# Kernel optimization log

Measured on AMD Instinct MI355X. Metric: run time of the kernel, lower is better.

## Reference

```python
import jax, jax.numpy as jnp
from jax import lax
import numpy as np

DIM = 48
HEADS = 2
HIDDEN = 96  # int(dim * 2.0)
EPS_LN = 1e-5
EPS_NORM = 1e-12


def _ln(x, w, b):
    # WithBias LayerNorm over channel dim (dim=1 in NCHW == last dim in b,(hw),c)
    mu = jnp.mean(x, axis=1, keepdims=True)
    var = jnp.var(x, axis=1, keepdims=True)
    return (x - mu) / jnp.sqrt(var + EPS_LN) * w[None, :, None, None] + b[None, :, None, None]


def _conv1x1(x, w, b):
    # w: [O, C, 1, 1]
    return jnp.einsum('bchw,oc->bohw', x, w[:, :, 0, 0]) + b[None, :, None, None]


def _dwconv3(x, w, b):
    # w: [C, 1, 3, 3], groups=C
    y = lax.conv_general_dilated(x, w, (1, 1), 'SAME',
                                 feature_group_count=x.shape[1],
                                 dimension_numbers=('NCHW', 'OIHW', 'NCHW'))
    return y + b[None, :, None, None]


def _l2norm(x):
    n = jnp.sqrt(jnp.sum(x * x, axis=-1, keepdims=True))
    return x / jnp.maximum(n, EPS_NORM)


def setup_inputs() -> dict:
    key = jax.random.key(0)
    ks = jax.random.split(key, 12)
    s = 0.02
    inp = {
        'x': jax.random.normal(ks[0], (2, DIM, 64, 64), jnp.float32),
        'norm1_w': jnp.ones((DIM,), jnp.float32),
        'norm1_b': jnp.zeros((DIM,), jnp.float32),
        'qkv_w': jax.random.normal(ks[1], (DIM * 3, DIM, 1, 1), jnp.float32) * s,
        'qkv_b': jnp.zeros((DIM * 3,), jnp.float32),
        'qkvdw_w': jax.random.normal(ks[2], (DIM * 3, 1, 3, 3), jnp.float32) * s,
        'qkvdw_b': jnp.zeros((DIM * 3,), jnp.float32),
        'temperature': jnp.ones((HEADS, 1, 1), jnp.float32),
        'proj_w': jax.random.normal(ks[3], (DIM, DIM, 1, 1), jnp.float32) * s,
        'proj_b': jnp.zeros((DIM,), jnp.float32),
        'norm2_w': jnp.ones((DIM,), jnp.float32),
        'norm2_b': jnp.zeros((DIM,), jnp.float32),
        'fi_w': jax.random.normal(ks[4], (HIDDEN * 2, DIM, 1, 1), jnp.float32) * s,
        'fi_b': jnp.zeros((HIDDEN * 2,), jnp.float32),
        'fdw_w': jax.random.normal(ks[5], (HIDDEN * 2, 1, 3, 3), jnp.float32) * s,
        'fdw_b': jnp.zeros((HIDDEN * 2,), jnp.float32),
        'fo_w': jax.random.normal(ks[6], (DIM, HIDDEN, 1, 1), jnp.float32) * s,
        'fo_b': jnp.zeros((DIM,), jnp.float32),
    }
    return inp


def _block(x, norm1_w, norm1_b, qkv_w, qkv_b, qkvdw_w, qkvdw_b, temperature,
           proj_w, proj_b, norm2_w, norm2_b, fi_w, fi_b, fdw_w, fdw_b, fo_w, fo_b):
    b, c, h, w = x.shape
    n = h * w
    chead = c // HEADS
    # --- attention branch ---
    xn = _ln(x, norm1_w, norm1_b)
    qkv = _dwconv3(_conv1x1(xn, qkv_w, qkv_b), qkvdw_w, qkvdw_b)
    q, k, v = jnp.split(qkv, 3, axis=1)
    def to_heads(t):  # [b, heads*chead, h, w] -> [b, heads, n, chead]
        return t.reshape(b, HEADS, chead, n).transpose(0, 1, 3, 2)
    q, k, v = to_heads(q), to_heads(k), to_heads(v)
    q = _l2norm(q)
    k = _l2norm(k)
    attn = jnp.einsum('bhnc,bhmc->bhnm', q, k) * temperature[None]
    attn = jax.nn.softmax(attn, axis=-1)
    out = jnp.einsum('bhnm,bhmc->bhnc', attn, v)
    out = out.transpose(0, 1, 3, 2).reshape(b, c, h, w)
    x = x + _conv1x1(out, proj_w, proj_b)
    # --- ffn branch ---
    xn = _ln(x, norm2_w, norm2_b)
    y = _dwconv3(_conv1x1(xn, fi_w, fi_b), fdw_w, fdw_b)
    y1, y2 = jnp.split(y, 2, axis=1)
    y = jax.nn.gelu(y1, approximate=False) * y2
    x = x + _conv1x1(y, fo_w, fo_b)
    return x


def reference(x, norm1_w, norm1_b, qkv_w, qkv_b, qkvdw_w, qkvdw_b, temperature,
              proj_w, proj_b, norm2_w, norm2_b, fi_w, fi_b, fdw_w, fdw_b, fo_w, fo_b):
    return _block(x, norm1_w, norm1_b, qkv_w, qkv_b, qkvdw_w, qkvdw_b, temperature,
                  proj_w, proj_b, norm2_w, norm2_b, fi_w, fi_b, fdw_w, fdw_b, fo_w, fo_b)
```

## Files before the change

kernel.cpp:

```cpp
#include <hip/hip_runtime.h>
#include <hip/hip_bf16.h>
#include <math.h>

#define NPIX 4096
#define NB 2

typedef __attribute__((ext_vector_type(8))) short short8;
typedef __attribute__((ext_vector_type(4))) float floatx4;

static __device__ inline short f2bf(float f) {
    union { float f; unsigned u; } v; v.f = f;
    unsigned r = (v.u + 0x7FFFu + ((v.u >> 16) & 1u)) >> 16;
    return (short)r;
}
static __device__ inline float bf2f(short s) {
    union { unsigned u; float f; } v;
    v.u = ((unsigned)(unsigned short)s) << 16;
    return v.f;
}
static __device__ inline unsigned pk2(float a, float b) {
    __hip_bfloat162 pk = __float22bfloat162_rn(make_float2(a, b));
    return *(unsigned*)&pk;
}

__global__ void k_prepw(const float* __restrict__ qkvw, const float* __restrict__ fiw,
                        const float* __restrict__ fow, const float* __restrict__ projw,
                        short* __restrict__ qkvwbf, short* __restrict__ fiwbf,
                        short* __restrict__ fowbf, short* __restrict__ projwbf) {
    int idx = blockIdx.x * 256 + threadIdx.x;
    if (idx < 144 * 64) {
        int o = idx >> 6, c = idx & 63;
        qkvwbf[idx] = (c < 48) ? f2bf(qkvw[o * 48 + c]) : (short)0;
        return;
    }
    idx -= 144 * 64;
    if (idx < 192 * 64) {
        int o = idx >> 6, c = idx & 63;
        fiwbf[idx] = (c < 48) ? f2bf(fiw[o * 48 + c]) : (short)0;
        return;
    }
    idx -= 192 * 64;
    if (idx < 48 * 96) {
        fowbf[idx] = f2bf(fow[idx]);
        return;
    }
    idx -= 48 * 96;
    if (idx < 48 * 64) {
        int o = idx >> 6, c = idx & 63;
        int h = c >> 5, cc = c & 31;
        projwbf[idx] = (cc < 24) ? f2bf(projw[o * 48 + h * 24 + cc]) : (short)0;
    }
}

__global__ __launch_bounds__(256) void k_qkv_fused(
    const float* __restrict__ xin, const float* __restrict__ n1w, const float* __restrict__ n1b,
    const short* __restrict__ qkvwbf, const float* __restrict__ qkvb,
    const float* __restrict__ dww, const float* __restrict__ dwb,
    const float* __restrict__ temp,
    short* __restrict__ Qbf, short* __restrict__ Kbf, short* __restrict__ Vbf)
{
    int px0 = blockIdx.x * 16;
    int y = blockIdx.y, b = blockIdx.z;
    int t = threadIdx.x;
    int w = t >> 6, lane = t & 63, l15 = lane & 15, quad = lane >> 4;

    __shared__ __align__(16) short xn[64][72];
    __shared__ short qkv[64][148];
    __shared__ float q2[16][148];
    __shared__ float red[4][64], redq[4][64];
    __shared__ float muS[64], rsS[64];
    __shared__ float dwwS[1296], dwbS[144];
    __shared__ short vmask[64];

    for (int u = t; u < 1296; u += 256) dwwS[u] = dww[u];
    if (t < 144) dwbS[t] = dwb[t];

    int pp = t & 63, cg2 = t >> 6;
    int rr = pp / 18, ix = pp - rr * 18;
    int yy = y + rr - 1, xpx = px0 - 1 + ix;
    bool pv = (pp < 54) && ((unsigned)yy < 64u) && ((unsigned)xpx < 64u);
    if (cg2 == 0) vmask[pp] = pv ? (short)1 : (short)0;

    float v[12]; float s = 0.f, sq = 0.f;
    if (pv) {
        size_t pbase = (size_t)(yy * 64 + xpx);
#pragma unroll
        for (int j2 = 0; j2 < 12; j2++) {
            float vv = xin[((size_t)b * 48 + cg2 * 12 + j2) * NPIX + pbase];
            v[j2] = vv; s += vv; sq += vv * vv;
        }
    } else {
#pragma unroll
        for (int j2 = 0; j2 < 12; j2++) v[j2] = 0.f;
    }
    red[cg2][pp] = s; redq[cg2][pp] = sq;
    __syncthreads();
    if (t < 64) {
        float ss = red[0][t] + red[1][t] + red[2][t] + red[3][t];
        float qq = redq[0][t] + redq[1][t] + redq[2][t] + redq[3][t];
        float mu = ss * (1.f / 48.f);
        float var = qq * (1.f / 48.f) - mu * mu;
        muS[t] = mu; rsS[t] = rsqrtf(var + 1e-5f);
    }
    __syncthreads();
    {
        float mu = muS[pp], rs = rsS[pp];
#pragma unroll
        for (int j2 = 0; j2 < 12; j2++) {
            int c = cg2 * 12 + j2;
            xn[pp][c] = f2bf((v[j2] - mu) * rs * n1w[c] + n1b[c]);
        }
        short8 z8 = {};
        if (cg2 == 0) *(short8*)&xn[pp][48] = z8;
        else if (cg2 == 1) *(short8*)&xn[pp][56] = z8;
    }
    __syncthreads();
    floatx4 zf = {0.f, 0.f, 0.f, 0.f};
    for (int job = w; job < 36; job += 4) {
        int pt = job / 9, ot = job % 9;
        short8 a0 = *(const short8*)&xn[pt * 16 + l15][quad * 8];
        short8 a1 = *(const short8*)&xn[pt * 16 + l15][32 + quad * 8];
        const short* wb = qkvwbf + (ot * 16 + l15) * 64;
        short8 b0 = *(const short8*)(wb + quad * 8);
        short8 b1 = *(const short8*)(wb + 32 + quad * 8);
        floatx4 c = __builtin_amdgcn_mfma_f32_16x16x32_bf16(a0, b0, zf, 0, 0, 0);
        c = __builtin_amdgcn_mfma_f32_16x16x32_bf16(a1, b1, c, 0, 0, 0);
        int oc = ot * 16 + l15;
        float bi = qkvb[oc];
#pragma unroll
        for (int r = 0; r < 4; r++) {
            int opp = pt * 16 + quad * 4 + r;
            qkv[opp][oc] = vmask[opp] ? f2bf(c[r] + bi) : (short)0;
        }
    }
    __syncthreads();
    {
        int i = t & 15, g3 = t >> 4;
        for (int cc = 0; cc < 9; cc++) {
            int c = g3 * 9 + cc;
            const float* wp = dwwS + c * 9;
            float acc = dwbS[c];
#pragma unroll
            for (int dy = 0; dy < 3; dy++)
#pragma unroll
                for (int dx = 0; dx < 3; dx++)
                    acc += bf2f(qkv[dy * 18 + i + dx][c]) * wp[dy * 3 + dx];
            q2[i][c] = acc;
        }
    }
    __syncthreads();
    if (t < 128) {
        int i = t & 15, h = (t >> 4) & 1, sel = t >> 5;
        int n = y * 64 + px0 + i;
        int bh = b * 2 + h;
        if (sel < 2) {
            float vv2[24]; float ss = 0.f;
            int base = sel * 48 + h * 24;
#pragma unroll
            for (int c = 0; c < 24; c++) { vv2[c] = q2[i][base + c]; ss += vv2[c] * vv2[c]; }
            float sc = ((sel == 0) ? temp[h] * 1.44269504089f : 1.f) / fmaxf(sqrtf(ss), 1e-12f);
            short qs[32];
#pragma unroll
            for (int c = 0; c < 24; c++) qs[c] = f2bf(vv2[c] * sc);
#pragma unroll
            for (int c = 24; c < 32; c++) qs[c] = 0;
            short* dst = ((sel == 0) ? Qbf : Kbf) + ((size_t)bh * NPIX + n) * 32;
#pragma unroll
            for (int i8 = 0; i8 < 4; i8++) {
                short8 st;
#pragma unroll
                for (int j2 = 0; j2 < 8; j2++) st[j2] = qs[i8 * 8 + j2];
                *(short8*)(dst + i8 * 8) = st;
            }
        } else {
            int half = sel - 2;
            int r5 = n & 31;
            int pos = (r5 < 16) ? ((r5 >> 2) * 8 + (r5 & 3))
                                : (((r5 & 15) >> 2) * 8 + (r5 & 3) + 4);
            int vcol = (n & ~31) + pos;
#pragma unroll
            for (int cc = 0; cc < 12; cc++) {
                int c = half * 12 + cc;
                Vbf[((size_t)bh * 32 + c) * NPIX + vcol] = f2bf(q2[i][96 + h * 24 + c]);
            }
            if (half == 1) {
#pragma unroll
                for (int c = 24; c < 32; c++)
                    Vbf[((size_t)bh * 32 + c) * NPIX + vcol] =
                        (c == 24) ? (short)0x3F80 : (short)0;
            }
        }
    }
}

__global__ __launch_bounds__(1024) void k_attn_mfma2(
    const short* __restrict__ Qbf, const short* __restrict__ Kbf,
    const short* __restrict__ Vbf, short* __restrict__ O)
{
    int qt = blockIdx.x, bh = blockIdx.y;
    int t = threadIdx.x;
    int tg = t & 255, g = t >> 8;
    int wloc = (t >> 6) & 3, lane = t & 63, l15 = lane & 15, quad = lane >> 4;

    __shared__ __align__(16) short tileK[4][2][64][40];
    __shared__ __align__(16) short tileV[4][2][32][72];
    __shared__ float Ocomb[4][64][33];

    int qrow0 = qt * 64 + wloc * 16;
    short8 bq = *(const short8*)(Qbf + ((size_t)bh * NPIX + qrow0 + l15) * 32 + quad * 8);

    int krow = tg >> 2, kseg = tg & 3;
    int vch = tg >> 3, vseg = tg & 7;
    const short* srcK = Kbf + ((size_t)bh * NPIX + krow) * 32 + kseg * 8;
    const short* srcV = Vbf + ((size_t)(bh * 32 + vch)) * NPIX + vseg * 8;

    int key0 = g * 1024;
    *(short8*)&tileK[g][0][krow][kseg * 8] = *(const short8*)(srcK + (size_t)key0 * 32);
    *(short8*)&tileV[g][0][vch][vseg * 8]  = *(const short8*)(srcV + key0);

    floatx4 zf = {0.f, 0.f, 0.f, 0.f};
    floatx4 o0 = zf, o1 = zf;

    const int NKT = 16;
    for (int kt = 0; kt < NKT; kt++) {
        __syncthreads();
        int cur = kt & 1;
        short8 ldK = {}, ldV = {};
        if (kt < NKT - 1) {
            int kabs = key0 + (kt + 1) * 64;
            ldK = *(const short8*)(srcK + (size_t)kabs * 32);
            ldV = *(const short8*)(srcV + kabs);
        }
        short8 ka0 = *(const short8*)&tileK[g][cur][l15][quad * 8];
        short8 ka1 = *(const short8*)&tileK[g][cur][16 + l15][quad * 8];
        short8 ka2 = *(const short8*)&tileK[g][cur][32 + l15][quad * 8];
        short8 ka3 = *(const short8*)&tileK[g][cur][48 + l15][quad * 8];
        floatx4 s0 = __builtin_amdgcn_mfma_f32_16x16x32_bf16(ka0, bq, zf, 0, 0, 0);
        floatx4 s1 = __builtin_amdgcn_mfma_f32_16x16x32_bf16(ka1, bq, zf, 0, 0, 0);
        floatx4 s2 = __builtin_amdgcn_mfma_f32_16x16x32_bf16(ka2, bq, zf, 0, 0, 0);
        floatx4 s3 = __builtin_amdgcn_mfma_f32_16x16x32_bf16(ka3, bq, zf, 0, 0, 0);
        float e0[4], e1[4], e2[4], e3[4];
#pragma unroll
        for (int r = 0; r < 4; r++) {
            e0[r] = exp2f(s0[r]); e1[r] = exp2f(s1[r]);
            e2[r] = exp2f(s2[r]); e3[r] = exp2f(s3[r]);
        }
        short8 p01, p23;
        {
            unsigned* u01 = (unsigned*)&p01;
            unsigned* u23 = (unsigned*)&p23;
            u01[0] = pk2(e0[0], e0[1]); u01[1] = pk2(e0[2], e0[3]);
            u01[2] = pk2(e1[0], e1[1]); u01[3] = pk2(e1[2], e1[3]);
            u23[0] = pk2(e2[0], e2[1]); u23[1] = pk2(e2[2], e2[3]);
            u23[2] = pk2(e3[0], e3[1]); u23[3] = pk2(e3[2], e3[3]);
        }
        short8 va00 = *(const short8*)&tileV[g][cur][l15][quad * 8];
        short8 va01 = *(const short8*)&tileV[g][cur][l15][32 + quad * 8];
        short8 va10 = *(const short8*)&tileV[g][cur][16 + l15][quad * 8];
        short8 va11 = *(const short8*)&tileV[g][cur][16 + l15][32 + quad * 8];
        o0 = __builtin_amdgcn_mfma_f32_16x16x32_bf16(va00, p01, o0, 0, 0, 0);
        o0 = __builtin_amdgcn_mfma_f32_16x16x32_bf16(va01, p23, o0, 0, 0, 0);
        o1 = __builtin_amdgcn_mfma_f32_16x16x32_bf16(va10, p01, o1, 0, 0, 0);
        o1 = __builtin_amdgcn_mfma_f32_16x16x32_bf16(va11, p23, o1, 0, 0, 0);
        if (kt < NKT - 1) {
            *(short8*)&tileK[g][1 - cur][krow][kseg * 8] = ldK;
            *(short8*)&tileV[g][1 - cur][vch][vseg * 8]  = ldV;
        }
    }
    int qi = wloc * 16 + l15;
#pragma unroll
    for (int r = 0; r < 4; r++) {
        Ocomb[g][qi][quad * 4 + r]      = o0[r];
        Ocomb[g][qi][16 + quad * 4 + r] = o1[r];
    }
    __syncthreads();
    {
        int qq = t >> 4, cp = t & 15;
        float l4 = Ocomb[0][qq][24] + Ocomb[1][qq][24] +
                   Ocomb[2][qq][24] + Ocomb[3][qq][24];
        float inv = 1.f / l4;
        float sa = (Ocomb[0][qq][2 * cp] + Ocomb[1][qq][2 * cp] +
                    Ocomb[2][qq][2 * cp] + Ocomb[3][qq][2 * cp]) * inv;
        float sb = (Ocomb[0][qq][2 * cp + 1] + Ocomb[1][qq][2 * cp + 1] +
                    Ocomb[2][qq][2 * cp + 1] + Ocomb[3][qq][2 * cp + 1]) * inv;
        int b = bh >> 1, h = bh & 1;
        int n = qt * 64 + qq;
        *(unsigned*)(O + ((size_t)b * NPIX + n) * 64 + h * 32 + 2 * cp) = pk2(sa, sb);
    }
}

__global__ __launch_bounds__(256) void k_tail_fused(
    const float* __restrict__ xin, const short* __restrict__ O,
    const short* __restrict__ projwbf, const float* __restrict__ projb,
    const float* __restrict__ n2w, const float* __restrict__ n2b,
    const short* __restrict__ fiwbf, const float* __restrict__ fib,
    const float* __restrict__ fdww, const float* __restrict__ fdwb,
    const short* __restrict__ fowbf, const float* __restrict__ fob,
    float* __restrict__ out)
{
    int px0 = blockIdx.x * 16;
    int y = blockIdx.y, b = blockIdx.z;
    int t = threadIdx.x;
    int w = t >> 6, lane = t & 63, l15 = lane & 15, quad = lane >> 4;

    __shared__ float x1s[64][53];
    __shared__ __align__(16) short xn2[64][72];
    __shared__ short ypre[56][196];
    __shared__ __align__(16) short yv[16][104];
    __shared__ float red[4][64], redq[4][64];
    __shared__ float muS[64], rsS[64];
    __shared__ float fdwwS[1728], fdwbS[192];
    __shared__ short vmask[64];
    __shared__ int nidx[64];

    for (int u = t; u < 1728; u += 256) fdwwS[u] = fdww[u];
    if (t < 192) fdwbS[t] = fdwb[t];
    if (t < 64) {
        int rr = t / 18, ix = t - rr * 18;
        int yy = y + rr - 1, xpx = px0 - 1 + ix;
        bool pv = (t < 54) && ((unsigned)yy < 64u) && ((unsigned)xpx < 64u);
        vmask[t] = pv ? (short)1 : (short)0;
        int n = yy * 64 + xpx;
        n = n < 0 ? 0 : (n > 4095 ? 4095 : n);
        nidx[t] = n;
    }
    __syncthreads();

    floatx4 zf = {0.f, 0.f, 0.f, 0.f};
    for (int job = w; job < 12; job += 4) {
        int pt = job / 3, ot = job % 3;
        const short* oa = O + ((size_t)b * NPIX + nidx[pt * 16 + l15]) * 64;
        short8 a0 = *(const short8*)(oa + quad * 8);
        short8 a1 = *(const short8*)(oa + 32 + quad * 8);
        const short* wb = projwbf + (ot * 16 + l15) * 64;
        short8 b0 = *(const short8*)(wb + quad * 8);
        short8 b1 = *(const short8*)(wb + 32 + quad * 8);
        floatx4 c = __builtin_amdgcn_mfma_f32_16x16x32_bf16(a0, b0, zf, 0, 0, 0);
        c = __builtin_amdgcn_mfma_f32_16x16x32_bf16(a1, b1, c, 0, 0, 0);
        int oc = ot * 16 + l15;
        float bi = projb[oc];
#pragma unroll
        for (int r = 0; r < 4; r++) {
            int opp = pt * 16 + quad * 4 + r;
            x1s[opp][oc] = xin[((size_t)b * 48 + oc) * NPIX + nidx[opp]] + c[r] + bi;
        }
    }
    __syncthreads();
    int pp = t & 63, cg2 = t >> 6;
    {
        float v[12]; float s = 0.f, sq = 0.f;
#pragma unroll
        for (int j2 = 0; j2 < 12; j2++) {
            float vv = x1s[pp][cg2 * 12 + j2];
            v[j2] = vv; s += vv; sq += vv * vv;
        }
        red[cg2][pp] = s; redq[cg2][pp] = sq;
        __syncthreads();
        if (t < 64) {
            float ss = red[0][t] + red[1][t] + red[2][t] + red[3][t];
            float qq = redq[0][t] + redq[1][t] + redq[2][t] + redq[3][t];
            float mu = ss * (1.f / 48.f);
            float var = qq * (1.f / 48.f) - mu * mu;
            muS[t] = mu; rsS[t] = rsqrtf(var + 1e-5f);
        }
        __syncthreads();
        float mu = muS[pp], rs = rsS[pp];
#pragma unroll
        for (int j2 = 0; j2 < 12; j2++) {
            int c = cg2 * 12 + j2;
            xn2[pp][c] = f2bf((v[j2] - mu) * rs * n2w[c] + n2b[c]);
        }
        short8 z8 = {};
        if (cg2 == 0) *(short8*)&xn2[pp][48] = z8;
        else if (cg2 == 1) *(short8*)&xn2[pp][56] = z8;
    }
    __syncthreads();
    for (int job = w; job < 48; job += 4) {
        int pt = job / 12, ot = job % 12;
        short8 a0 = *(const short8*)&xn2[pt * 16 + l15][quad * 8];
        short8 a1 = *(const short8*)&xn2[pt * 16 + l15][32 + quad * 8];
        const short* wb = fiwbf + (ot * 16 + l15) * 64;
        short8 b0 = *(const short8*)(wb + quad * 8);
        short8 b1 = *(const short8*)(wb + 32 + quad * 8);
        floatx4 c = __builtin_amdgcn_mfma_f32_16x16x32_bf16(a0, b0, zf, 0, 0, 0);
        c = __builtin_amdgcn_mfma_f32_16x16x32_bf16(a1, b1, c, 0, 0, 0);
        int oc = ot * 16 + l15;
        float bi = fib[oc];
#pragma unroll
        for (int r = 0; r < 4; r++) {
            int opp = pt * 16 + quad * 4 + r;
            if (opp < 56) ypre[opp][oc] = vmask[opp] ? f2bf(c[r] + bi) : (short)0;
        }
    }
    __syncthreads();
    {
        int i = t & 15, gg = t >> 4;
        for (int cc = 0; cc < 6; cc++) {
            int c = gg * 6 + cc;
            const float* wp  = fdwwS + c * 9;
            const float* wp2 = fdwwS + (c + 96) * 9;
            float a = fdwbS[c], g2v = fdwbS[c + 96];
#pragma unroll
            for (int dy = 0; dy < 3; dy++)
#pragma unroll
                for (int dx = 0; dx < 3; dx++) {
                    int ppi = dy * 18 + i + dx;
                    a   += bf2f(ypre[ppi][c])      * wp[dy * 3 + dx];
                    g2v += bf2f(ypre[ppi][c + 96]) * wp2[dy * 3 + dx];
                }
            float ge = 0.5f * a * (1.f + erff(a * 0.70710678118654752f));
            yv[i][c] = f2bf(ge * g2v);
        }
        short8 z8 = {};
        if (gg == 0) *(short8*)&yv[i][96] = z8;
    }
    __syncthreads();
    if (w < 3) {
        floatx4 c = zf;
#pragma unroll
        for (int k = 0; k < 3; k++) {
            short8 a  = *(const short8*)&yv[l15][k * 32 + quad * 8];
            short8 bb = *(const short8*)(fowbf + (w * 16 + l15) * 96 + k * 32 + quad * 8);
            c = __builtin_amdgcn_mfma_f32_16x16x32_bf16(a, bb, c, 0, 0, 0);
        }
        int oc = w * 16 + l15;
        float bi = fob[oc];
#pragma unroll
        for (int r = 0; r < 4; r++) {
            int i = quad * 4 + r;
            size_t idx = ((size_t)b * 48 + oc) * NPIX + y * 64 + px0 + i;
            out[idx] = x1s[19 + i][oc] + c[r] + bi;
        }
    }
}

extern "C" void kernel_launch(void* const* d_in, const int* in_sizes, int n_in,
                              void* d_out, int out_size, void* d_ws, size_t ws_size,
                              hipStream_t stream) {
    const float* x       = (const float*)d_in[0];
    const float* n1w     = (const float*)d_in[1];
    const float* n1b     = (const float*)d_in[2];
    const float* qkv_w   = (const float*)d_in[3];
    const float* qkv_b   = (const float*)d_in[4];
    const float* qkvdw_w = (const float*)d_in[5];
    const float* qkvdw_b = (const float*)d_in[6];
    const float* temp    = (const float*)d_in[7];
    const float* proj_w  = (const float*)d_in[8];
    const float* proj_b  = (const float*)d_in[9];
    const float* n2w     = (const float*)d_in[10];
    const float* n2b     = (const float*)d_in[11];
    const float* fi_w    = (const float*)d_in[12];
    const float* fi_b    = (const float*)d_in[13];
    const float* fdw_w   = (const float*)d_in[14];
    const float* fdw_b   = (const float*)d_in[15];
    const float* fo_w    = (const float*)d_in[16];
    const float* fo_b    = (const float*)d_in[17];

    short* sws = (short*)d_ws;
    short* Qbf     = sws;
    short* Kbf     = Qbf + 524288;
    short* Vbf     = Kbf + 524288;
    short* Obuf    = Vbf + 524288;
    short* qkvwbf  = Obuf + 524288;
    short* fiwbf   = qkvwbf + 9216;
    short* fowbf   = fiwbf + 12288;
    short* projwbf = fowbf + 4608;

    {
        int total = 144 * 64 + 192 * 64 + 48 * 96 + 48 * 64;
        k_prepw<<<(total + 255) / 256, 256, 0, stream>>>(qkv_w, fi_w, fo_w, proj_w,
                                                         qkvwbf, fiwbf, fowbf, projwbf);
    }
    {
        dim3 g(4, 64, NB);
        k_qkv_fused<<<g, 256, 0, stream>>>(x, n1w, n1b, qkvwbf, qkv_b,
                                           qkvdw_w, qkvdw_b, temp, Qbf, Kbf, Vbf);
    }
    {
        dim3 g(64, 4);
        k_attn_mfma2<<<g, 1024, 0, stream>>>(Qbf, Kbf, Vbf, Obuf);
    }
    {
        dim3 g(4, 64, NB);
        k_tail_fused<<<g, 256, 0, stream>>>(x, Obuf, projwbf, proj_b, n2w, n2b,
                                            fiwbf, fi_b, fdw_w, fdw_b, fowbf, fo_b,
                                            (float*)d_out);
    }
}
```

Measured before the change: 148.3 us.

## Restructure attention kernel to load K/V directly into registers with double buffering

Replaces the 1024-thread attention kernel, which staged K/V tiles through shared memory behind per-iteration barriers, with a 256-thread kernel. Each wave loads K and V fragments straight from global memory into registers, double-buffered across two key tiles. Each wave handles 32 query rows, so every loaded K/V fragment is reused for two query sub-tiles. This removes LDS traffic and most __syncthreads calls, and the launch grid grows to 128x4 blocks. In exchange it raises register pressure and relies on the cache to serve the strided V loads.

```diff
diff --git a/kernel.cpp b/kernel.cpp
--- a/kernel.cpp
+++ b/kernel.cpp
@@ -193,99 +193,102 @@
     }
 }
 
-__global__ __launch_bounds__(1024) void k_attn_mfma2(
+__global__ __launch_bounds__(256) void k_attn_mfma3(
     const short* __restrict__ Qbf, const short* __restrict__ Kbf,
     const short* __restrict__ Vbf, short* __restrict__ O)
 {
-    int qt = blockIdx.x, bh = blockIdx.y;
+    int qt32 = blockIdx.x, bh = blockIdx.y;
     int t = threadIdx.x;
-    int tg = t & 255, g = t >> 8;
-    int wloc = (t >> 6) & 3, lane = t & 63, l15 = lane & 15, quad = lane >> 4;
-
-    __shared__ __align__(16) short tileK[4][2][64][40];
-    __shared__ __align__(16) short tileV[4][2][32][72];
-    __shared__ float Ocomb[4][64][33];
-
-    int qrow0 = qt * 64 + wloc * 16;
-    short8 bq = *(const short8*)(Qbf + ((size_t)bh * NPIX + qrow0 + l15) * 32 + quad * 8);
-
-    int krow = tg >> 2, kseg = tg & 3;
-    int vch = tg >> 3, vseg = tg & 7;
-    const short* srcK = Kbf + ((size_t)bh * NPIX + krow) * 32 + kseg * 8;
-    const short* srcV = Vbf + ((size_t)(bh * 32 + vch)) * NPIX + vseg * 8;
-
-    int key0 = g * 1024;
-    *(short8*)&tileK[g][0][krow][kseg * 8] = *(const short8*)(srcK + (size_t)key0 * 32);
-    *(short8*)&tileV[g][0][vch][vseg * 8]  = *(const short8*)(srcV + key0);
+    int w = t >> 6, lane = t & 63, l15 = lane & 15, quad = lane >> 4;
+
+    __shared__ float Ocomb[4][32][33];
+
+    int qrow0 = qt32 * 32;
+    short8 bq0 = *(const short8*)(Qbf + ((size_t)bh * NPIX + qrow0 + l15) * 32 + quad * 8);
+    short8 bq1 = *(const short8*)(Qbf + ((size_t)bh * NPIX + qrow0 + 16 + l15) * 32 + quad * 8);
+    const short* Kb = Kbf + (size_t)bh * NPIX * 32;
+    const short* Vb = Vbf + (size_t)bh * 32 * NPIX;
 
     floatx4 zf = {0.f, 0.f, 0.f, 0.f};
-    floatx4 o0 = zf, o1 = zf;
-
-    const int NKT = 16;
-    for (int kt = 0; kt < NKT; kt++) {
-        __syncthreads();
-        int cur = kt & 1;
-        short8 ldK = {}, ldV = {};
-        if (kt < NKT - 1) {
-            int kabs = key0 + (kt + 1) * 64;
-            ldK = *(const short8*)(srcK + (size_t)kabs * 32);
-            ldV = *(const short8*)(srcV + kabs);
-        }
-        short8 ka0 = *(const short8*)&tileK[g][cur][l15][quad * 8];
-        short8 ka1 = *(const short8*)&tileK[g][cur][16 + l15][quad * 8];
-        short8 ka2 = *(const short8*)&tileK[g][cur][32 + l15][quad * 8];
-        short8 ka3 = *(const short8*)&tileK[g][cur][48 + l15][quad * 8];
-        floatx4 s0 = __builtin_amdgcn_mfma_f32_16x16x32_bf16(ka0, bq, zf, 0, 0, 0);
-        floatx4 s1 = __builtin_amdgcn_mfma_f32_16x16x32_bf16(ka1, bq, zf, 0, 0, 0);
-        floatx4 s2 = __builtin_amdgcn_mfma_f32_16x16x32_bf16(ka2, bq, zf, 0, 0, 0);
-        floatx4 s3 = __builtin_amdgcn_mfma_f32_16x16x32_bf16(ka3, bq, zf, 0, 0, 0);
-        float e0[4], e1[4], e2[4], e3[4];
-#pragma unroll
-        for (int r = 0; r < 4; r++) {
-            e0[r] = exp2f(s0[r]); e1[r] = exp2f(s1[r]);
-            e2[r] = exp2f(s2[r]); e3[r] = exp2f(s3[r]);
-        }
-        short8 p01, p23;
-        {
-            unsigned* u01 = (unsigned*)&p01;
-            unsigned* u23 = (unsigned*)&p23;
-            u01[0] = pk2(e0[0], e0[1]); u01[1] = pk2(e0[2], e0[3]);
-            u01[2] = pk2(e1[0], e1[1]); u01[3] = pk2(e1[2], e1[3]);
-            u23[0] = pk2(e2[0], e2[1]); u23[1] = pk2(e2[2], e2[3]);
-            u23[2] = pk2(e3[0], e3[1]); u23[3] = pk2(e3[2], e3[3]);
-        }
-        short8 va00 = *(const short8*)&tileV[g][cur][l15][quad * 8];
-        short8 va01 = *(const short8*)&tileV[g][cur][l15][32 + quad * 8];
-        short8 va10 = *(const short8*)&tileV[g][cur][16 + l15][quad * 8];
-        short8 va11 = *(const short8*)&tileV[g][cur][16 + l15][32 + quad * 8];
-        o0 = __builtin_amdgcn_mfma_f32_16x16x32_bf16(va00, p01, o0, 0, 0, 0);
-        o0 = __builtin_amdgcn_mfma_f32_16x16x32_bf16(va01, p23, o0, 0, 0, 0);
-        o1 = __builtin_amdgcn_mfma_f32_16x16x32_bf16(va10, p01, o1, 0, 0, 0);
-        o1 = __builtin_amdgcn_mfma_f32_16x16x32_bf16(va11, p23, o1, 0, 0, 0);
-        if (kt < NKT - 1) {
-            *(short8*)&tileK[g][1 - cur][krow][kseg * 8] = ldK;
-            *(short8*)&tileV[g][1 - cur][vch][vseg * 8]  = ldV;
-        }
-    }
-    int qi = wloc * 16 + l15;
+    floatx4 o00 = zf, o01 = zf, o10 = zf, o11 = zf;
+    int key0 = w * 1024;
+
+#define LOADK(kabs, K0, K1, K2, K3) \
+    K0 = *(const short8*)(Kb + (size_t)((kabs) + l15) * 32 + quad * 8); \
+    K1 = *(const short8*)(Kb + (size_t)((kabs) + 16 + l15) * 32 + quad * 8); \
+    K2 = *(const short8*)(Kb + (size_t)((kabs) + 32 + l15) * 32 + quad * 8); \
+    K3 = *(const short8*)(Kb + (size_t)((kabs) + 48 + l15) * 32 + quad * 8);
+#define LOADV(kabs, V0, V1, V2, V3) \
+    V0 = *(const short8*)(Vb + (size_t)l15 * NPIX + (kabs) + quad * 8); \
+    V1 = *(const short8*)(Vb + (size_t)l15 * NPIX + (kabs) + 32 + quad * 8); \
+    V2 = *(const short8*)(Vb + (size_t)(16 + l15) * NPIX + (kabs) + quad * 8); \
+    V3 = *(const short8*)(Vb + (size_t)(16 + l15) * NPIX + (kabs) + 32 + quad * 8);
+
+#define QSET(K0, K1, K2, K3, V0, V1, V2, V3, BQ, OA, OB) { \
+    floatx4 s0 = __builtin_amdgcn_mfma_f32_16x16x32_bf16(K0, BQ, zf, 0, 0, 0); \
+    floatx4 s1 = __builtin_amdgcn_mfma_f32_16x16x32_bf16(K1, BQ, zf, 0, 0, 0); \
+    floatx4 s2 = __builtin_amdgcn_mfma_f32_16x16x32_bf16(K2, BQ, zf, 0, 0, 0); \
+    floatx4 s3 = __builtin_amdgcn_mfma_f32_16x16x32_bf16(K3, BQ, zf, 0, 0, 0); \
+    short8 p01, p23; \
+    { unsigned* u01 = (unsigned*)&p01; unsigned* u23 = (unsigned*)&p23; \
+      u01[0] = pk2(exp2f(s0[0]), exp2f(s0[1])); u01[1] = pk2(exp2f(s0[2]), exp2f(s0[3])); \
+      u01[2] = pk2(exp2f(s1[0]), exp2f(s1[1])); u01[3] = pk2(exp2f(s1[2]), exp2f(s1[3])); \
+      u23[0] = pk2(exp2f(s2[0]), exp2f(s2[1])); u23[1] = pk2(exp2f(s2[2]), exp2f(s2[3])); \
+      u23[2] = pk2(exp2f(s3[0]), exp2f(s3[1])); u23[3] = pk2(exp2f(s3[2]), exp2f(s3[3])); } \
+    OA = __builtin_amdgcn_mfma_f32_16x16x32_bf16(V0, p01, OA, 0, 0, 0); \
+    OA = __builtin_amdgcn_mfma_f32_16x16x32_bf16(V1, p23, OA, 0, 0, 0); \
+    OB = __builtin_amdgcn_mfma_f32_16x16x32_bf16(V2, p01, OB, 0, 0, 0); \
+    OB = __builtin_amdgcn_mfma_f32_16x16x32_bf16(V3, p23, OB, 0, 0, 0); }
+
+#define COMPUTE(K0, K1, K2, K3, V0, V1, V2, V3) \
+    QSET(K0, K1, K2, K3, V0, V1, V2, V3, bq0, o00, o01) \
+    QSET(K0, K1, K2, K3, V0, V1, V2, V3, bq1, o10, o11)
+
+    short8 ka0, ka1, ka2, ka3, va0, va1, va2, va3;
+    short8 kb0, kb1, kb2, kb3, vb0, vb1, vb2, vb3;
+    LOADK(key0, ka0, ka1, ka2, ka3)
+    LOADV(key0, va0, va1, va2, va3)
+    for (int kt2 = 0; kt2 < 8; kt2++) {
+        int kn = key0 + (kt2 * 2 + 1) * 64;
+        LOADK(kn, kb0, kb1, kb2, kb3)
+        LOADV(kn, vb0, vb1, vb2, vb3)
+        COMPUTE(ka0, ka1, ka2, ka3, va0, va1, va2, va3)
+        if (kt2 < 7) {
+            int kn2 = key0 + (kt2 * 2 + 2) * 64;
+            LOADK(kn2, ka0, ka1, ka2, ka3)
+            LOADV(kn2, va0, va1, va2, va3)
+        }
+        COMPUTE(kb0, kb1, kb2, kb3, vb0, vb1, vb2, vb3)
+    }
+#undef LOADK
+#undef LOADV
+#undef QSET
+#undef COMPUTE
+
 #pragma unroll
     for (int r = 0; r < 4; r++) {
-        Ocomb[g][qi][quad * 4 + r]      = o0[r];
-        Ocomb[g][qi][16 + quad * 4 + r] = o1[r];
-    }
-    __syncthreads();
-    {
-        int qq = t >> 4, cp = t & 15;
+        Ocomb[w][l15][quad * 4 + r]           = o00[r];
+        Ocomb[w][l15][16 + quad * 4 + r]      = o01[r];
+        Ocomb[w][16 + l15][quad * 4 + r]      = o10[r];
+        Ocomb[w][16 + l15][16 + quad * 4 + r] = o11[r];
+    }
+    __syncthreads();
+    {
+        int qq = t >> 3, cp0 = t & 7;
         float l4 = Ocomb[0][qq][24] + Ocomb[1][qq][24] +
                    Ocomb[2][qq][24] + Ocomb[3][qq][24];
         float inv = 1.f / l4;
-        float sa = (Ocomb[0][qq][2 * cp] + Ocomb[1][qq][2 * cp] +
-                    Ocomb[2][qq][2 * cp] + Ocomb[3][qq][2 * cp]) * inv;
-        float sb = (Ocomb[0][qq][2 * cp + 1] + Ocomb[1][qq][2 * cp + 1] +
-                    Ocomb[2][qq][2 * cp + 1] + Ocomb[3][qq][2 * cp + 1]) * inv;
-        int b = bh >> 1, h = bh & 1;
-        int n = qt * 64 + qq;
-        *(unsigned*)(O + ((size_t)b * NPIX + n) * 64 + h * 32 + 2 * cp) = pk2(sa, sb);
+        int b2 = bh >> 1, h = bh & 1;
+        int n = qrow0 + qq;
+#pragma unroll
+        for (int half = 0; half < 2; half++) {
+            int cp = cp0 + half * 8;
+            float sa = (Ocomb[0][qq][2 * cp] + Ocomb[1][qq][2 * cp] +
+                        Ocomb[2][qq][2 * cp] + Ocomb[3][qq][2 * cp]) * inv;
+            float sb = (Ocomb[0][qq][2 * cp + 1] + Ocomb[1][qq][2 * cp + 1] +
+                        Ocomb[2][qq][2 * cp + 1] + Ocomb[3][qq][2 * cp + 1]) * inv;
+            *(unsigned*)(O + ((size_t)b2 * NPIX + n) * 64 + h * 32 + 2 * cp) = pk2(sa, sb);
+        }
     }
 }
 
@@ -477,8 +480,8 @@
                                            qkvdw_w, qkvdw_b, temp, Qbf, Kbf, Vbf);
     }
     {
-        dim3 g(64, 4);
-        k_attn_mfma2<<<g, 1024, 0, stream>>>(Qbf, Kbf, Vbf, Obuf);
+        dim3 g(128, 4);
+        k_attn_mfma3<<<g, 256, 0, stream>>>(Qbf, Kbf, Vbf, Obuf);
     }
     {
         dim3 g(4, 64, NB);
```

Result: slower. 152.1 us (+2.6%).
